# Performance work log

Hardware: AMD Instinct MI355X
Metric: run time of the kernel (lower is better)

## Reference

```python
import jax, jax.numpy as jnp
import numpy as np

NUM_HEADS = 8  # from init_kwargs
SR = 2         # sr_ratio from init_kwargs


def layernorm(t, g, b, eps=1e-5):
    mu = jnp.mean(t, axis=-1, keepdims=True)
    var = jnp.mean((t - mu) ** 2, axis=-1, keepdims=True)
    return (t - mu) * jax.lax.rsqrt(var + eps) * g + b


def setup_inputs() -> dict:
    key = jax.random.key(0)
    ks = jax.random.split(key, 6)
    B, C = 4, 256
    Hx = Wx = 64
    Hz = Wz = 32
    N = Hz * Wz + Hx * Wx  # 5120 (template tokens first, then search tokens)
    s = 0.02
    return {
        "x": jax.random.normal(ks[0], (B, N, C), jnp.float32),
        "Wq": jax.random.normal(ks[1], (C, C), jnp.float32) * s,          # nn.Linear(dim, dim, bias=False)
        "Wkv": jax.random.normal(ks[2], (2 * C, C), jnp.float32) * s,     # nn.Linear(dim, 2*dim, bias=False)
        "Wsr": jax.random.normal(ks[3], (C, C, SR, SR), jnp.float32) * s, # Conv2d(dim, dim, k=sr, stride=sr) OIHW
        "bsr": jnp.zeros((C,), jnp.float32),
        "gamma": jnp.ones((C,), jnp.float32),
        "beta": jnp.zeros((C,), jnp.float32),
        "Wproj": jax.random.normal(ks[4], (C, C), jnp.float32) * s,
        "bproj": jnp.zeros((C,), jnp.float32),
        "H_x": Hx, "W_x": Wx, "H_z": Hz, "W_z": Wz,
    }


def reference(x, Wq, Wkv, Wsr, bsr, gamma, beta, Wproj, bproj, H_x, W_x, H_z, W_z):
    B, N, C = x.shape
    h = NUM_HEADS
    d = C // h
    scale = d ** -0.5
    Nz, Nx = H_z * W_z, H_x * W_x

    # q for all tokens: [B, h, N, d]
    q = (x @ Wq.T).reshape(B, N, h, d).transpose(0, 2, 1, 3)

    # spatial reduction (sr_ratio > 1 branch): strided conv + layernorm on each stream
    z_tok, x_tok = x[:, :Nz], x[:, Nz:]
    ker = jnp.transpose(Wsr, (2, 3, 1, 0))  # OIHW -> HWIO

    def sr_branch(t, H, W):
        img = t.reshape(B, H, W, C)  # NHWC; same layout as torch NCHW reshape
        out = jax.lax.conv_general_dilated(
            img, ker, window_strides=(SR, SR), padding="VALID",
            dimension_numbers=("NHWC", "HWIO", "NHWC")) + bsr
        out = out.reshape(B, -1, C)
        return layernorm(out, gamma, beta)

    x_ = sr_branch(x_tok, H_x, W_x)  # [B, (Hx/sr)*(Wx/sr), C]
    z_ = sr_branch(z_tok, H_z, W_z)  # [B, (Hz/sr)*(Wz/sr), C]
    zL = z_.shape[1]
    cat = jnp.concatenate([z_, x_], axis=1)  # [B, L, C]

    kv = (cat @ Wkv.T).reshape(B, -1, 2, h, d).transpose(2, 0, 3, 1, 4)  # [2, B, h, L, d]
    k, v = kv[0], kv[1]

    q_z, q_x = q[:, :, :Nz], q[:, :, Nz:]
    k_z, v_z = k[:, :, :zL], v[:, :, :zL]

    # template queries attend only to reduced template keys/values
    attn_z = jax.nn.softmax(jnp.einsum("bhqd,bhkd->bhqk", q_z, k_z) * scale, axis=-1)
    out_z = jnp.einsum("bhqk,bhkd->bhqd", attn_z, v_z).transpose(0, 2, 1, 3).reshape(B, Nz, C)

    # search queries attend to full (template+search) reduced keys/values
    attn_x = jax.nn.softmax(jnp.einsum("bhqd,bhkd->bhqk", q_x, k) * scale, axis=-1)
    out_x = jnp.einsum("bhqk,bhkd->bhqd", attn_x, v).transpose(0, 2, 1, 3).reshape(B, Nx, C)

    out = jnp.concatenate([out_z, out_x], axis=1)
    return out @ Wproj.T + bproj
```

## Files before the change

kernel.cpp:

```cpp
#include <hip/hip_runtime.h>
#include <hip/hip_bf16.h>
#include <cstddef>

#define BATCH 4
#define CCH 256
#define NHEAD 8
#define DHEAD 32
#define NZ 1024
#define NX 4096
#define NTOK 5120
#define LKV 1280
#define SCALE 0.17677669529663687f
#define QC 0.25503486f

typedef __attribute__((ext_vector_type(8))) short bf16x8;
typedef __attribute__((ext_vector_type(4))) float floatx4;

__device__ inline short f2bf(float f) {
  __hip_bfloat16 h = __float2bfloat16(f);
  return __builtin_bit_cast(short, h);
}
__device__ inline unsigned int pk2(float a, float b) {
  unsigned int lo = (unsigned short)f2bf(a);
  unsigned int hi = (unsigned short)f2bf(b);
  return lo | (hi << 16);
}

__global__ __launch_bounds__(256) void cvt_bf16(const float* __restrict__ src,
                                                short* __restrict__ dst, int n8) {
  int i = blockIdx.x * 256 + threadIdx.x;
  if (i >= n8) return;
  float4 v0 = ((const float4*)src)[i * 2];
  float4 v1 = ((const float4*)src)[i * 2 + 1];
  uint4 u;
  u.x = pk2(v0.x, v0.y); u.y = pk2(v0.z, v0.w);
  u.z = pk2(v1.x, v1.y); u.w = pk2(v1.z, v1.w);
  ((uint4*)dst)[i] = u;
}

__global__ __launch_bounds__(256) void reorder_wsr(const float* __restrict__ Wsr,
                                                   short* __restrict__ Wkb) {
  int i = blockIdx.x * 256 + threadIdx.x;
  int co = i >> 10;
  int rem = i & 1023;
  int di = rem >> 9, dj = (rem >> 8) & 1, ci = rem & 255;
  Wkb[i] = f2bf(Wsr[((co * 256 + ci) * 2 + di) * 2 + dj]);
}

__global__ __launch_bounds__(256) void im2col_kernel(const short* __restrict__ xbf,
                                                     short* __restrict__ patch) {
  int blk = blockIdx.x;
  int b = blk / 1280, t = blk % 1280;
  int c = threadIdx.x;
#pragma unroll
  for (int di = 0; di < 2; ++di)
#pragma unroll
    for (int dj = 0; dj < 2; ++dj) {
      int src;
      if (t < 256) {
        int oi = t >> 4, oj = t & 15;
        src = b * NTOK + (2 * oi + di) * 32 + (2 * oj + dj);
      } else {
        int tt = t - 256;
        int oi = tt >> 5, oj = tt & 31;
        src = b * NTOK + NZ + (2 * oi + di) * 64 + (2 * oj + dj);
      }
      patch[(size_t)blk * 1024 + di * 512 + dj * 256 + c] = xbf[(size_t)src * CCH + c];
    }
}

#define MG_PROLOG()                                                          \
  __shared__ short As[64][72];                                               \
  __shared__ short Bs[64][72];                                               \
  int bm = blockIdx.y * 64, bn = blockIdx.x * 64;                            \
  int tid = threadIdx.x;                                                     \
  int wave = tid >> 6, lane = tid & 63, lg = lane >> 4, lr = lane & 15;      \
  int sr = tid >> 2, sc = tid & 3;                                           \
  floatx4 acc[4] = {{0.f,0.f,0.f,0.f},{0.f,0.f,0.f,0.f},                     \
                    {0.f,0.f,0.f,0.f},{0.f,0.f,0.f,0.f}};                    \
  (void)lane;

#define MG_LOOP(Abf, Bbf, K)                                                 \
  for (int k0 = 0; k0 < (K); k0 += 64) {                                     \
    bf16x8 a0 = *(const bf16x8*)&(Abf)[(size_t)(bm + sr) * (K) + k0 + sc * 8];       \
    bf16x8 a1 = *(const bf16x8*)&(Abf)[(size_t)(bm + sr) * (K) + k0 + (sc + 4) * 8]; \
    bf16x8 b0 = *(const bf16x8*)&(Bbf)[(size_t)(bn + sr) * (K) + k0 + sc * 8];       \
    bf16x8 b1 = *(const bf16x8*)&(Bbf)[(size_t)(bn + sr) * (K) + k0 + (sc + 4) * 8]; \
    __syncthreads();                                                         \
    *(bf16x8*)&As[sr][sc * 8] = a0;                                          \
    *(bf16x8*)&As[sr][(sc + 4) * 8] = a1;                                    \
    *(bf16x8*)&Bs[sr][sc * 8] = b0;                                          \
    *(bf16x8*)&Bs[sr][(sc + 4) * 8] = b1;                                    \
    __syncthreads();                                                         \
    bf16x8 af0 = *(bf16x8*)&As[wave * 16 + lr][lg * 8];                      \
    bf16x8 af1 = *(bf16x8*)&As[wave * 16 + lr][32 + lg * 8];                 \
    _Pragma("unroll") for (int n = 0; n < 4; ++n) {                          \
      bf16x8 bf0 = *(bf16x8*)&Bs[n * 16 + lr][lg * 8];                       \
      bf16x8 bf1 = *(bf16x8*)&Bs[n * 16 + lr][32 + lg * 8];                  \
      acc[n] = __builtin_amdgcn_mfma_f32_16x16x32_bf16(af0, bf0, acc[n], 0, 0, 0); \
      acc[n] = __builtin_amdgcn_mfma_f32_16x16x32_bf16(af1, bf1, acc[n], 0, 0, 0); \
    }                                                                        \
  }

__global__ __launch_bounds__(256) void gemm_q(const short* __restrict__ A,
                                              const short* __restrict__ Bm,
                                              short* __restrict__ qbf) {
  MG_PROLOG()
  MG_LOOP(A, Bm, 256)
#pragma unroll
  for (int n = 0; n < 4; ++n) {
    int c = bn + 16 * n + lr;
    int h = c >> 5, d = c & 31;
#pragma unroll
    for (int reg = 0; reg < 4; ++reg) {
      int m = bm + wave * 16 + 4 * lg + reg;
      int b = m / NTOK, tok = m - b * NTOK;
      qbf[((size_t)(b * 8 + h) * NTOK + tok) * 32 + d] = f2bf(acc[n][reg] * QC);
    }
  }
}

__global__ __launch_bounds__(256) void gemm_conv(const short* __restrict__ A,
                                                 const short* __restrict__ Bm,
                                                 float* __restrict__ Cm) {
  MG_PROLOG()
  MG_LOOP(A, Bm, 1024)
#pragma unroll
  for (int n = 0; n < 4; ++n) {
    int c = bn + 16 * n + lr;
#pragma unroll
    for (int reg = 0; reg < 4; ++reg) {
      int m = bm + wave * 16 + 4 * lg + reg;
      Cm[(size_t)m * 256 + c] = acc[n][reg];
    }
  }
}

__global__ __launch_bounds__(256) void gemm_kv(const short* __restrict__ A,
                                               const short* __restrict__ Bm,
                                               short* __restrict__ Kbf,
                                               short* __restrict__ Vtb) {
  MG_PROLOG()
  MG_LOOP(A, Bm, 256)
#pragma unroll
  for (int n = 0; n < 4; ++n) {
    int c = bn + 16 * n + lr;
#pragma unroll
    for (int reg = 0; reg < 4; ++reg) {
      int m = bm + wave * 16 + 4 * lg + reg;
      int b = m / LKV, kvg = m - b * LKV;
      if (c < 256) {
        int h = c >> 5, d = c & 31;
        Kbf[((size_t)(b * 8 + h) * LKV + kvg) * 32 + d] = f2bf(acc[n][reg]);
      } else {
        int cc = c - 256;
        int h = cc >> 5, d = cc & 31;
        int tile = kvg >> 6, kvin = kvg & 63;
        Vtb[(((size_t)(b * 8 + h) * 20 + tile) * 32 + d) * 64 + kvin] = f2bf(acc[n][reg]);
      }
    }
  }
}

__global__ __launch_bounds__(256) void ln_kernel(const float* __restrict__ cat_pre,
                                                 const float* __restrict__ bsr,
                                                 const float* __restrict__ gamma,
                                                 const float* __restrict__ beta,
                                                 short* __restrict__ catb) {
  int row = blockIdx.x * 4 + (threadIdx.x >> 6);
  int lane = threadIdx.x & 63;
  float4 v = *(const float4*)&cat_pre[(size_t)row * 256 + lane * 4];
  float4 bb = *(const float4*)&bsr[lane * 4];
  v.x += bb.x; v.y += bb.y; v.z += bb.z; v.w += bb.w;
  float s = (v.x + v.y) + (v.z + v.w);
#pragma unroll
  for (int mask = 1; mask < 64; mask <<= 1) s += __shfl_xor(s, mask, 64);
  float mu = s * (1.f / 256.f);
  float4 dv;
  dv.x = v.x - mu; dv.y = v.y - mu; dv.z = v.z - mu; dv.w = v.w - mu;
  float q = dv.x * dv.x + dv.y * dv.y + dv.z * dv.z + dv.w * dv.w;
#pragma unroll
  for (int mask = 1; mask < 64; mask <<= 1) q += __shfl_xor(q, mask, 64);
  float rs = rsqrtf(q * (1.f / 256.f) + 1e-5f);
  float4 g = *(const float4*)&gamma[lane * 4];
  float4 be = *(const float4*)&beta[lane * 4];
  uint2 st;
  st.x = pk2(dv.x * rs * g.x + be.x, dv.y * rs * g.y + be.y);
  st.y = pk2(dv.z * rs * g.z + be.z, dv.w * rs * g.w + be.w);
  *(uint2*)&catb[(size_t)row * 256 + lane * 4] = st;
}

__global__ __launch_bounds__(256) void attn_mfma(const short* __restrict__ qbf,
                                                 const short* __restrict__ Kbf,
                                                 const short* __restrict__ Vtb,
                                                 float* __restrict__ out,
                                                 int q0, int kvlen, int tshift) {
  int bh = blockIdx.x >> tshift;
  int qt = blockIdx.x & ((1 << tshift) - 1);
  int b = bh >> 3, hh = bh & 7;
  int tid = threadIdx.x;
  int wave = tid >> 6, lane = tid & 63, lg = lane >> 4, lr = lane & 15;

  __shared__ short Ps[4][64][72];

  int qtok = q0 + qt * 256 + wave * 64;
  const short* qb = qbf + ((size_t)bh * NTOK + qtok) * 32;
  bf16x8 qf[4];
#pragma unroll
  for (int qi = 0; qi < 4; ++qi)
    qf[qi] = *(const bf16x8*)&qb[(16 * qi + lr) * 32 + lg * 8];

  const short* Kb = Kbf + (size_t)bh * LKV * 32;
  const short* Vb = Vtb + (size_t)bh * 20 * 2048;

  floatx4 oacc[4][2];
#pragma unroll
  for (int qi = 0; qi < 4; ++qi)
#pragma unroll
    for (int n = 0; n < 2; ++n) oacc[qi][n] = (floatx4){0.f, 0.f, 0.f, 0.f};
  float lsum[4] = {0.f, 0.f, 0.f, 0.f};

  bf16x8 kfc[4], vfc[2][2];
#pragma unroll
  for (int m = 0; m < 4; ++m)
    kfc[m] = *(const bf16x8*)&Kb[(size_t)(16 * m + lr) * 32 + lg * 8];
#pragma unroll
  for (int n = 0; n < 2; ++n)
#pragma unroll
    for (int kb = 0; kb < 2; ++kb)
      vfc[n][kb] = *(const bf16x8*)&Vb[(16 * n + lr) * 64 + kb * 32 + lg * 8];

  for (int l0 = 0; l0 < kvlen; l0 += 64) {
#pragma unroll
    for (int qi = 0; qi < 4; ++qi) {
      floatx4 st[4];
#pragma unroll
      for (int m = 0; m < 4; ++m)
        st[m] = __builtin_amdgcn_mfma_f32_16x16x32_bf16(
            kfc[m], qf[qi], (floatx4){0.f, 0.f, 0.f, 0.f}, 0, 0, 0);
      int pr = 16 * qi + lr;
#pragma unroll
      for (int m = 0; m < 4; ++m) {
        float p0 = __builtin_amdgcn_exp2f(st[m][0]);
        float p1 = __builtin_amdgcn_exp2f(st[m][1]);
        float p2 = __builtin_amdgcn_exp2f(st[m][2]);
        float p3 = __builtin_amdgcn_exp2f(st[m][3]);
        lsum[qi] += (p0 + p1) + (p2 + p3);
        *(unsigned int*)&Ps[wave][pr][16 * m + 4 * lg]     = pk2(p0, p1);
        *(unsigned int*)&Ps[wave][pr][16 * m + 4 * lg + 2] = pk2(p2, p3);
      }
    }

    bf16x8 kfn[4], vfn[2][2];
    int l1 = l0 + 64;
    if (l1 < kvlen) {
      const short* Vbt = Vb + (l1 >> 6) * 2048;
#pragma unroll
      for (int m = 0; m < 4; ++m)
        kfn[m] = *(const bf16x8*)&Kb[(size_t)(l1 + 16 * m + lr) * 32 + lg * 8];
#pragma unroll
      for (int n = 0; n < 2; ++n)
#pragma unroll
        for (int kb = 0; kb < 2; ++kb)
          vfn[n][kb] = *(const bf16x8*)&Vbt[(16 * n + lr) * 64 + kb * 32 + lg * 8];
    }

#pragma unroll
    for (int qi = 0; qi < 4; ++qi)
#pragma unroll
      for (int kb = 0; kb < 2; ++kb) {
        bf16x8 pf = *(bf16x8*)&Ps[wave][16 * qi + lr][kb * 32 + lg * 8];
#pragma unroll
        for (int n = 0; n < 2; ++n)
          oacc[qi][n] = __builtin_amdgcn_mfma_f32_16x16x32_bf16(pf, vfc[n][kb], oacc[qi][n], 0, 0, 0);
      }

#pragma unroll
    for (int m = 0; m < 4; ++m) kfc[m] = kfn[m];
#pragma unroll
    for (int n = 0; n < 2; ++n)
#pragma unroll
      for (int kb = 0; kb < 2; ++kb) vfc[n][kb] = vfn[n][kb];
  }

#pragma unroll
  for (int qi = 0; qi < 4; ++qi) {
    lsum[qi] += __shfl_xor(lsum[qi], 16, 64);
    lsum[qi] += __shfl_xor(lsum[qi], 32, 64);
  }

#pragma unroll
  for (int qi = 0; qi < 4; ++qi)
#pragma unroll
    for (int reg = 0; reg < 4; ++reg) {
      float lv = __shfl(lsum[qi], 4 * lg + reg, 64);
      float inv = 1.f / lv;
      int gr = b * NTOK + qtok + 16 * qi + 4 * lg + reg;
      float* ob = out + (size_t)gr * CCH + hh * DHEAD;
      ob[lr]      = oacc[qi][0][reg] * inv;
      ob[16 + lr] = oacc[qi][1][reg] * inv;
    }
}

#define BM 64
#define BN 64
#define BK 16
__global__ __launch_bounds__(256) void gemm_nt(const float* __restrict__ A,
                                               const float* __restrict__ Bm,
                                               const float* __restrict__ bias,
                                               float* __restrict__ Cm,
                                               int M, int N, int K) {
  __shared__ float As[BK][BM + 4];
  __shared__ float Bs[BK][BN + 4];
  int bm = blockIdx.y * BM, bn = blockIdx.x * BN;
  int tid = threadIdx.x;
  int tm = (tid >> 4) << 2;
  int tn = (tid & 15) << 2;
  int lr = tid >> 2;
  int lq = tid & 3;
  const float* Aptr = A + (size_t)(bm + lr) * K + lq * 4;
  const float* Bptr = Bm + (size_t)(bn + lr) * K + lq * 4;
  float acc[4][4];
#pragma unroll
  for (int i = 0; i < 4; ++i)
#pragma unroll
    for (int j = 0; j < 4; ++j) acc[i][j] = 0.f;

  for (int k0 = 0; k0 < K; k0 += BK) {
    float4 av = *(const float4*)(Aptr + k0);
    float4 bv = *(const float4*)(Bptr + k0);
    __syncthreads();
    As[lq * 4 + 0][lr] = av.x; As[lq * 4 + 1][lr] = av.y;
    As[lq * 4 + 2][lr] = av.z; As[lq * 4 + 3][lr] = av.w;
    Bs[lq * 4 + 0][lr] = bv.x; Bs[lq * 4 + 1][lr] = bv.y;
    Bs[lq * 4 + 2][lr] = bv.z; Bs[lq * 4 + 3][lr] = bv.w;
    __syncthreads();
#pragma unroll
    for (int kk = 0; kk < BK; ++kk) {
      float4 a4 = *(const float4*)&As[kk][tm];
      float4 b4 = *(const float4*)&Bs[kk][tn];
      float aa[4] = {a4.x, a4.y, a4.z, a4.w};
      float bb[4] = {b4.x, b4.y, b4.z, b4.w};
#pragma unroll
      for (int i = 0; i < 4; ++i)
#pragma unroll
        for (int j = 0; j < 4; ++j) acc[i][j] += aa[i] * bb[j];
    }
  }
#pragma unroll
  for (int i = 0; i < 4; ++i) {
    float4 o;
    o.x = acc[i][0] + bias[bn + tn + 0];
    o.y = acc[i][1] + bias[bn + tn + 1];
    o.z = acc[i][2] + bias[bn + tn + 2];
    o.w = acc[i][3] + bias[bn + tn + 3];
    *(float4*)(Cm + (size_t)(bm + tm + i) * N + bn + tn) = o;
  }
}

extern "C" void kernel_launch(void* const* d_in, const int* in_sizes, int n_in,
                              void* d_out, int out_size, void* d_ws, size_t ws_size,
                              hipStream_t stream) {
  (void)in_sizes; (void)n_in; (void)out_size; (void)ws_size;
  const float* x     = (const float*)d_in[0];
  const float* Wq    = (const float*)d_in[1];
  const float* Wkv   = (const float*)d_in[2];
  const float* Wsr   = (const float*)d_in[3];
  const float* bsr   = (const float*)d_in[4];
  const float* gamma = (const float*)d_in[5];
  const float* beta  = (const float*)d_in[6];
  const float* Wproj = (const float*)d_in[7];
  const float* bproj = (const float*)d_in[8];
  float* out = (float*)d_out;
  float* ws  = (float*)d_ws;

  short* qbf      = (short*)ws;
  float* attn_out = ws + 2621440;
  short* patch    = (short*)(ws + 2621440);
  short* xbf      = (short*)(ws + 7864320);
  float* cat_pre  = ws + 10485760;
  short* catb     = (short*)(ws + 11796480);
  short* Kbf      = (short*)(ws + 12451840);
  short* Vtb      = (short*)(ws + 13107200);
  short* Wqb      = (short*)(ws + 13762560);
  short* Wkvb     = (short*)(ws + 13795328);
  short* Wkb      = (short*)(ws + 13860864);

  cvt_bf16<<<2560, 256, 0, stream>>>(x, xbf, 655360);
  cvt_bf16<<<32, 256, 0, stream>>>(Wq, Wqb, 8192);
  cvt_bf16<<<64, 256, 0, stream>>>(Wkv, Wkvb, 16384);
  reorder_wsr<<<1024, 256, 0, stream>>>(Wsr, Wkb);
  im2col_kernel<<<BATCH * LKV, 256, 0, stream>>>(xbf, patch);
  gemm_q<<<dim3(4, 320), 256, 0, stream>>>(xbf, Wqb, qbf);
  gemm_conv<<<dim3(4, 80), 256, 0, stream>>>(patch, Wkb, cat_pre);
  ln_kernel<<<1280, 256, 0, stream>>>(cat_pre, bsr, gamma, beta, catb);
  gemm_kv<<<dim3(8, 80), 256, 0, stream>>>(catb, Wkvb, Kbf, Vtb);
  attn_mfma<<<32 * 4, 256, 0, stream>>>(qbf, Kbf, Vtb, attn_out, 0, 256, 2);
  attn_mfma<<<32 * 16, 256, 0, stream>>>(qbf, Kbf, Vtb, attn_out, NZ, LKV, 4);
  gemm_nt<<<dim3(4, 320), 256, 0, stream>>>(attn_out, Wproj, bproj, out, BATCH * NTOK, 256, 256);
}
```

Before: 229.4 us.

## Use MFMA bf16 GEMM for output projection and merge attention launches

Replaces the fp32 scalar projection GEMM with a bf16 MFMA GEMM reusing the existing macro-based tile loop. Attention now writes bf16 output, which halves the intermediate traffic. The two attention launches are merged into one grid with smaller 32-row-per-wave tiles, giving more blocks and better occupancy. The probability packing also switches to a cheaper round-via-add-and-perm conversion. The cost is extra bf16 rounding on the attention output and projection weights, and the new packing skips proper round-to-nearest-even.

```diff
diff --git a/kernel.cpp b/kernel.cpp
--- a/kernel.cpp
+++ b/kernel.cpp
@@ -10,7 +10,6 @@
 #define NX 4096
 #define NTOK 5120
 #define LKV 1280
-#define SCALE 0.17677669529663687f
 #define QC 0.25503486f
 
 typedef __attribute__((ext_vector_type(8))) short bf16x8;
@@ -24,6 +23,11 @@
   unsigned int lo = (unsigned short)f2bf(a);
   unsigned int hi = (unsigned short)f2bf(b);
   return lo | (hi << 16);
+}
+__device__ inline unsigned int pk2f(float a, float b) {
+  unsigned int ua = __builtin_bit_cast(unsigned int, a) + 0x8000u;
+  unsigned int ub = __builtin_bit_cast(unsigned int, b) + 0x8000u;
+  return __builtin_amdgcn_perm(ub, ua, 0x07060302u);
 }
 
 __global__ __launch_bounds__(256) void cvt_bf16(const float* __restrict__ src,
@@ -162,6 +166,24 @@
   }
 }
 
+__global__ __launch_bounds__(256) void gemm_proj(const short* __restrict__ A,
+                                                 const short* __restrict__ Bm,
+                                                 const float* __restrict__ bias,
+                                                 float* __restrict__ Cm) {
+  MG_PROLOG()
+  MG_LOOP(A, Bm, 256)
+#pragma unroll
+  for (int n = 0; n < 4; ++n) {
+    int c = bn + 16 * n + lr;
+    float bv = bias[c];
+#pragma unroll
+    for (int reg = 0; reg < 4; ++reg) {
+      int m = bm + wave * 16 + 4 * lg + reg;
+      Cm[(size_t)m * 256 + c] = acc[n][reg] + bv;
+    }
+  }
+}
+
 __global__ __launch_bounds__(256) void ln_kernel(const float* __restrict__ cat_pre,
                                                  const float* __restrict__ bsr,
                                                  const float* __restrict__ gamma,
@@ -190,35 +212,40 @@
   *(uint2*)&catb[(size_t)row * 256 + lane * 4] = st;
 }
 
-__global__ __launch_bounds__(256) void attn_mfma(const short* __restrict__ qbf,
-                                                 const short* __restrict__ Kbf,
-                                                 const short* __restrict__ Vtb,
-                                                 float* __restrict__ out,
-                                                 int q0, int kvlen, int tshift) {
-  int bh = blockIdx.x >> tshift;
-  int qt = blockIdx.x & ((1 << tshift) - 1);
+__global__ __launch_bounds__(256) void attn_fused(const short* __restrict__ qbf,
+                                                  const short* __restrict__ Kbf,
+                                                  const short* __restrict__ Vtb,
+                                                  short* __restrict__ attn_out) {
+  int blk = blockIdx.x;
+  int bh, q0, kvlen;
+  if (blk < 1024) {
+    bh = blk >> 5; q0 = NZ + (blk & 31) * 128; kvlen = LKV;
+  } else {
+    int idx = blk - 1024;
+    bh = idx >> 3; q0 = (idx & 7) * 128; kvlen = 256;
+  }
   int b = bh >> 3, hh = bh & 7;
   int tid = threadIdx.x;
   int wave = tid >> 6, lane = tid & 63, lg = lane >> 4, lr = lane & 15;
 
-  __shared__ short Ps[4][64][72];
-
-  int qtok = q0 + qt * 256 + wave * 64;
+  __shared__ short Ps[4][32][72];
+
+  int qtok = q0 + wave * 32;
   const short* qb = qbf + ((size_t)bh * NTOK + qtok) * 32;
-  bf16x8 qf[4];
-#pragma unroll
-  for (int qi = 0; qi < 4; ++qi)
+  bf16x8 qf[2];
+#pragma unroll
+  for (int qi = 0; qi < 2; ++qi)
     qf[qi] = *(const bf16x8*)&qb[(16 * qi + lr) * 32 + lg * 8];
 
   const short* Kb = Kbf + (size_t)bh * LKV * 32;
   const short* Vb = Vtb + (size_t)bh * 20 * 2048;
 
-  floatx4 oacc[4][2];
-#pragma unroll
-  for (int qi = 0; qi < 4; ++qi)
+  floatx4 oacc[2][2];
+#pragma unroll
+  for (int qi = 0; qi < 2; ++qi)
 #pragma unroll
     for (int n = 0; n < 2; ++n) oacc[qi][n] = (floatx4){0.f, 0.f, 0.f, 0.f};
-  float lsum[4] = {0.f, 0.f, 0.f, 0.f};
+  float lsum[2] = {0.f, 0.f};
 
   bf16x8 kfc[4], vfc[2][2];
 #pragma unroll
@@ -232,7 +259,7 @@
 
   for (int l0 = 0; l0 < kvlen; l0 += 64) {
 #pragma unroll
-    for (int qi = 0; qi < 4; ++qi) {
+    for (int qi = 0; qi < 2; ++qi) {
       floatx4 st[4];
 #pragma unroll
       for (int m = 0; m < 4; ++m)
@@ -246,8 +273,8 @@
         float p2 = __builtin_amdgcn_exp2f(st[m][2]);
         float p3 = __builtin_amdgcn_exp2f(st[m][3]);
         lsum[qi] += (p0 + p1) + (p2 + p3);
-        *(unsigned int*)&Ps[wave][pr][16 * m + 4 * lg]     = pk2(p0, p1);
-        *(unsigned int*)&Ps[wave][pr][16 * m + 4 * lg + 2] = pk2(p2, p3);
+        *(unsigned int*)&Ps[wave][pr][16 * m + 4 * lg]     = pk2f(p0, p1);
+        *(unsigned int*)&Ps[wave][pr][16 * m + 4 * lg + 2] = pk2f(p2, p3);
       }
     }
 
@@ -266,7 +293,7 @@
     }
 
 #pragma unroll
-    for (int qi = 0; qi < 4; ++qi)
+    for (int qi = 0; qi < 2; ++qi)
 #pragma unroll
       for (int kb = 0; kb < 2; ++kb) {
         bf16x8 pf = *(bf16x8*)&Ps[wave][16 * qi + lr][kb * 32 + lg * 8];
@@ -284,78 +311,22 @@
   }
 
 #pragma unroll
-  for (int qi = 0; qi < 4; ++qi) {
+  for (int qi = 0; qi < 2; ++qi) {
     lsum[qi] += __shfl_xor(lsum[qi], 16, 64);
     lsum[qi] += __shfl_xor(lsum[qi], 32, 64);
   }
 
 #pragma unroll
-  for (int qi = 0; qi < 4; ++qi)
+  for (int qi = 0; qi < 2; ++qi)
 #pragma unroll
     for (int reg = 0; reg < 4; ++reg) {
       float lv = __shfl(lsum[qi], 4 * lg + reg, 64);
       float inv = 1.f / lv;
       int gr = b * NTOK + qtok + 16 * qi + 4 * lg + reg;
-      float* ob = out + (size_t)gr * CCH + hh * DHEAD;
-      ob[lr]      = oacc[qi][0][reg] * inv;
-      ob[16 + lr] = oacc[qi][1][reg] * inv;
-    }
-}
-
-#define BM 64
-#define BN 64
-#define BK 16
-__global__ __launch_bounds__(256) void gemm_nt(const float* __restrict__ A,
-                                               const float* __restrict__ Bm,
-                                               const float* __restrict__ bias,
-                                               float* __restrict__ Cm,
-                                               int M, int N, int K) {
-  __shared__ float As[BK][BM + 4];
-  __shared__ float Bs[BK][BN + 4];
-  int bm = blockIdx.y * BM, bn = blockIdx.x * BN;
-  int tid = threadIdx.x;
-  int tm = (tid >> 4) << 2;
-  int tn = (tid & 15) << 2;
-  int lr = tid >> 2;
-  int lq = tid & 3;
-  const float* Aptr = A + (size_t)(bm + lr) * K + lq * 4;
-  const float* Bptr = Bm + (size_t)(bn + lr) * K + lq * 4;
-  float acc[4][4];
-#pragma unroll
-  for (int i = 0; i < 4; ++i)
-#pragma unroll
-    for (int j = 0; j < 4; ++j) acc[i][j] = 0.f;
-
-  for (int k0 = 0; k0 < K; k0 += BK) {
-    float4 av = *(const float4*)(Aptr + k0);
-    float4 bv = *(const float4*)(Bptr + k0);
-    __syncthreads();
-    As[lq * 4 + 0][lr] = av.x; As[lq * 4 + 1][lr] = av.y;
-    As[lq * 4 + 2][lr] = av.z; As[lq * 4 + 3][lr] = av.w;
-    Bs[lq * 4 + 0][lr] = bv.x; Bs[lq * 4 + 1][lr] = bv.y;
-    Bs[lq * 4 + 2][lr] = bv.z; Bs[lq * 4 + 3][lr] = bv.w;
-    __syncthreads();
-#pragma unroll
-    for (int kk = 0; kk < BK; ++kk) {
-      float4 a4 = *(const float4*)&As[kk][tm];
-      float4 b4 = *(const float4*)&Bs[kk][tn];
-      float aa[4] = {a4.x, a4.y, a4.z, a4.w};
-      float bb[4] = {b4.x, b4.y, b4.z, b4.w};
-#pragma unroll
-      for (int i = 0; i < 4; ++i)
-#pragma unroll
-        for (int j = 0; j < 4; ++j) acc[i][j] += aa[i] * bb[j];
-    }
-  }
-#pragma unroll
-  for (int i = 0; i < 4; ++i) {
-    float4 o;
-    o.x = acc[i][0] + bias[bn + tn + 0];
-    o.y = acc[i][1] + bias[bn + tn + 1];
-    o.z = acc[i][2] + bias[bn + tn + 2];
-    o.w = acc[i][3] + bias[bn + tn + 3];
-    *(float4*)(Cm + (size_t)(bm + tm + i) * N + bn + tn) = o;
-  }
+      short* ob = attn_out + (size_t)gr * CCH + hh * DHEAD;
+      ob[lr]      = f2bf(oacc[qi][0][reg] * inv);
+      ob[16 + lr] = f2bf(oacc[qi][1][reg] * inv);
+    }
 }
 
 extern "C" void kernel_launch(void* const* d_in, const int* in_sizes, int n_in,
@@ -375,8 +346,8 @@
   float* ws  = (float*)d_ws;
 
   short* qbf      = (short*)ws;
-  float* attn_out = ws + 2621440;
-  short* patch    = (short*)(ws + 2621440);
+  short* attn_out = (short*)(ws + 2621440);
+  short* patch    = (short*)(ws + 5242880);
   short* xbf      = (short*)(ws + 7864320);
   float* cat_pre  = ws + 10485760;
   short* catb     = (short*)(ws + 11796480);
@@ -385,17 +356,18 @@
   short* Wqb      = (short*)(ws + 13762560);
   short* Wkvb     = (short*)(ws + 13795328);
   short* Wkb      = (short*)(ws + 13860864);
+  short* Wprojb   = (short*)(ws + 13991936);
 
   cvt_bf16<<<2560, 256, 0, stream>>>(x, xbf, 655360);
   cvt_bf16<<<32, 256, 0, stream>>>(Wq, Wqb, 8192);
   cvt_bf16<<<64, 256, 0, stream>>>(Wkv, Wkvb, 16384);
+  cvt_bf16<<<32, 256, 0, stream>>>(Wproj, Wprojb, 8192);
   reorder_wsr<<<1024, 256, 0, stream>>>(Wsr, Wkb);
   im2col_kernel<<<BATCH * LKV, 256, 0, stream>>>(xbf, patch);
   gemm_q<<<dim3(4, 320), 256, 0, stream>>>(xbf, Wqb, qbf);
   gemm_conv<<<dim3(4, 80), 256, 0, stream>>>(patch, Wkb, cat_pre);
   ln_kernel<<<1280, 256, 0, stream>>>(cat_pre, bsr, gamma, beta, catb);
   gemm_kv<<<dim3(8, 80), 256, 0, stream>>>(catb, Wkvb, Kbf, Vtb);
-  attn_mfma<<<32 * 4, 256, 0, stream>>>(qbf, Kbf, Vtb, attn_out, 0, 256, 2);
-  attn_mfma<<<32 * 16, 256, 0, stream>>>(qbf, Kbf, Vtb, attn_out, NZ, LKV, 4);
-  gemm_nt<<<dim3(4, 320), 256, 0, stream>>>(attn_out, Wproj, bproj, out, BATCH * NTOK, 256, 256);
-}
+  attn_fused<<<1280, 256, 0, stream>>>(qbf, Kbf, Vtb, attn_out);
+  gemm_proj<<<dim3(4, 320), 256, 0, stream>>>(attn_out, Wprojb, bproj, out);
+}
```

Measured after the change: 217.1 us. -5.3%, faster.
